# Kernel optimization log

Hardware: AMD Instinct MI355X
Metric: run time of the kernel (lower is better)

Reference implementation:

```python
import jax, jax.numpy as jnp
import numpy as np

N_NODES = 40000
N_EDGES = 640000
HIDDEN = 128
NUM_RBF = 50
CUTOFF = 10.0


def setup_inputs() -> dict:
    key = jax.random.key(0)
    ks = jax.random.split(key, 8)
    s = 1.0 / np.sqrt(HIDDEN)
    sf = 1.0 / np.sqrt(NUM_RBF)
    return {
        "x": jax.random.normal(ks[0], (N_NODES, HIDDEN), dtype=jnp.float32),
        "edge_index": jax.random.randint(ks[1], (2, N_EDGES), 0, N_NODES, dtype=jnp.int64),
        "edge_weight": jax.random.uniform(ks[2], (N_EDGES,), dtype=jnp.float32) * CUTOFF,
        "edge_attr": jax.random.normal(ks[3], (N_EDGES, NUM_RBF), dtype=jnp.float32),
        "W_f1": jax.random.normal(ks[4], (NUM_RBF, HIDDEN), dtype=jnp.float32) * sf,
        "b_f1": jnp.zeros((HIDDEN,), dtype=jnp.float32),
        "W_f2": jax.random.normal(ks[5], (HIDDEN, HIDDEN), dtype=jnp.float32) * s,
        "b_f2": jnp.zeros((HIDDEN,), dtype=jnp.float32),
        "W_in": jax.random.normal(ks[6], (HIDDEN, HIDDEN), dtype=jnp.float32) * s,
        "W_out": jax.random.normal(ks[7], (HIDDEN, HIDDEN), dtype=jnp.float32) * s,
        "b_out": jnp.zeros((HIDDEN,), dtype=jnp.float32),
        "W_lin": jax.random.normal(jax.random.fold_in(key, 7), (HIDDEN, HIDDEN), dtype=jnp.float32) * s,
        "b_lin": jnp.zeros((HIDDEN,), dtype=jnp.float32),
    }


def reference(x, edge_index, edge_weight, edge_attr,
              W_f1, b_f1, W_f2, b_f2, W_in, W_out, b_out, W_lin, b_lin):
    src = edge_index[0]
    dst = edge_index[1]
    n_nodes = x.shape[0]
    # filter network: MLP on RBF-expanded distances, modulated by cosine cutoff
    C = 0.5 * (jnp.cos(edge_weight * (jnp.pi / CUTOFF)) + 1.0)  # [E]
    Wf = jnp.tanh(edge_attr @ W_f1 + b_f1) @ W_f2 + b_f2        # [E, H]
    Wf = Wf * C[:, None]
    # cfconv: project, gather, filter-multiply, scatter-add, project
    h = x @ W_in                                                 # [N, H] (no bias)
    msg = h[src] * Wf                                            # [E, H]
    agg = jax.ops.segment_sum(msg, dst, num_segments=n_nodes)   # [N, H]
    out = agg @ W_out + b_out
    # interaction block tail: activation + linear
    out = jnp.tanh(out)
    return out @ W_lin + b_lin
```

## Files before the change

### kernel.cpp

```cpp
#include <hip/hip_runtime.h>
#include <hip/hip_bf16.h>

#define N_NODES 40000
#define N_EDGES 640000
#define HIDDEN  128
#define NUM_RBF 50
#define NBLK_SCAN 157

typedef __attribute__((ext_vector_type(8))) short bf16x8;
typedef __attribute__((ext_vector_type(4))) float f32x4;

#define WAVE_FENCE() do { asm volatile("" ::: "memory"); \
                          __builtin_amdgcn_sched_barrier(0); } while (0)

__device__ __forceinline__ short f2bf(float f) {
  __hip_bfloat16 h = __float2bfloat16(f);
  return (short)__builtin_bit_cast(unsigned short, h);
}
__device__ __forceinline__ float bf2f(unsigned short u) {
  unsigned int v = ((unsigned int)u) << 16;
  return __builtin_bit_cast(float, v);
}
__device__ __forceinline__ float bflo(unsigned int u) {
  return __builtin_bit_cast(float, u << 16);
}
__device__ __forceinline__ float bfhi(unsigned int u) {
  return __builtin_bit_cast(float, u & 0xffff0000u);
}
__device__ __forceinline__ unsigned int pack2bf(float a, float b) {
  return (unsigned int)(unsigned short)f2bf(a) |
         ((unsigned int)(unsigned short)f2bf(b) << 16);
}

__device__ __forceinline__ float fast_tanh(float x) {
  float e = __expf(2.0f * x);
  return 1.0f - 2.0f * __builtin_amdgcn_rcpf(e + 1.0f);
}

__device__ __forceinline__ f32x4 mfma16(bf16x8 a, bf16x8 b, f32x4 c) {
  return __builtin_amdgcn_mfma_f32_16x16x32_bf16(a, b, c, 0, 0, 0);
}

__device__ __forceinline__ bf16x8 load8_f32_bf16(const float* p) {
  const float4 v0 = ((const float4*)p)[0];
  const float4 v1 = ((const float4*)p)[1];
  bf16x8 r;
  r[0] = f2bf(v0.x); r[1] = f2bf(v0.y); r[2] = f2bf(v0.z); r[3] = f2bf(v0.w);
  r[4] = f2bf(v1.x); r[5] = f2bf(v1.y); r[6] = f2bf(v1.z); r[7] = f2bf(v1.w);
  return r;
}

__global__ __launch_bounds__(256) void hist_kernel(const int* __restrict__ ei,
                                                   int* __restrict__ hist) {
  int e = blockIdx.x * 256 + threadIdx.x;
  if (e < N_EDGES) atomicAdd(&hist[ei[N_EDGES + e]], 1);
}

__global__ __launch_bounds__(256) void scan1_kernel(const int* __restrict__ hist,
                                                    int* __restrict__ tmp,
                                                    int* __restrict__ bsum) {
  __shared__ int ls[256];
  const int t = threadIdx.x;
  const int i = blockIdx.x * 256 + t;
  int v = (i < N_NODES) ? hist[i] : 0;
  ls[t] = v;
  __syncthreads();
  for (int off = 1; off < 256; off <<= 1) {
    int u = (t >= off) ? ls[t - off] : 0;
    __syncthreads();
    ls[t] += u;
    __syncthreads();
  }
  if (i < N_NODES) tmp[i] = ls[t];
  if (t == 255) bsum[blockIdx.x] = ls[255];
}

__global__ __launch_bounds__(256) void scan2_kernel(const int* __restrict__ bsum,
                                                    int* __restrict__ bpfx,
                                                    int* __restrict__ row_start) {
  __shared__ int ls[256];
  const int t = threadIdx.x;
  int v = (t < NBLK_SCAN) ? bsum[t] : 0;
  ls[t] = v;
  __syncthreads();
  for (int off = 1; off < 256; off <<= 1) {
    int u = (t >= off) ? ls[t - off] : 0;
    __syncthreads();
    ls[t] += u;
    __syncthreads();
  }
  if (t < NBLK_SCAN) bpfx[t] = ls[t] - v;
  if (t == 255) row_start[N_NODES] = ls[255];
}

__global__ __launch_bounds__(256) void scan3_kernel(const int* __restrict__ hist,
                                                    const int* __restrict__ tmp,
                                                    const int* __restrict__ bpfx,
                                                    int* __restrict__ row_start,
                                                    int* __restrict__ cursor) {
  const int i = blockIdx.x * 256 + threadIdx.x;
  if (i < N_NODES) {
    int rs = tmp[i] - hist[i] + bpfx[blockIdx.x];
    row_start[i] = rs;
    cursor[i] = rs;
  }
}

__global__ __launch_bounds__(256) void perm_kernel(
    const int* __restrict__ ei, const float* __restrict__ ew,
    int* __restrict__ cursor,
    int* __restrict__ eSorted, int* __restrict__ srcSorted,
    float* __restrict__ Carr) {
  int e = blockIdx.x * 256 + threadIdx.x;
  if (e < N_EDGES) {
    int dst = ei[N_EDGES + e];
    int pos = atomicAdd(&cursor[dst], 1);
    eSorted[pos] = e;
    srcSorted[pos] = ei[e];
    Carr[pos] = 0.5f * (__cosf(ew[e] * 0.31415926535f) + 1.0f);
  }
}

__global__ __launch_bounds__(256) void hproj_kernel(
    const float* __restrict__ x, const float* __restrict__ W_in,
    unsigned short* __restrict__ hb)
{
  __shared__ __align__(16) unsigned short sWt[128 * 136];
  const int tid = threadIdx.x, wave = tid >> 6, lane = tid & 63;
  const int ln = lane & 15, grp = lane >> 4;
  const int r0 = blockIdx.x * 64;

  for (int idx = tid; idx < 128 * 128; idx += 256) {
    int k = idx >> 7, c = idx & 127;
    sWt[c * 136 + k] = f2bf(W_in[idx]);
  }
  __syncthreads();

  const size_t r = (size_t)r0 + wave * 16 + ln;
  f32x4 acc[8];
#pragma unroll
  for (int ct = 0; ct < 8; ++ct) acc[ct] = (f32x4){0.f, 0.f, 0.f, 0.f};
#pragma unroll
  for (int ks = 0; ks < 4; ++ks) {
    bf16x8 a = load8_f32_bf16(&x[r * 128 + ks * 32 + grp * 8]);
#pragma unroll
    for (int ct = 0; ct < 8; ++ct) {
      bf16x8 b = *(const bf16x8*)&sWt[(ct * 16 + ln) * 136 + ks * 32 + grp * 8];
      acc[ct] = mfma16(a, b, acc[ct]);
    }
  }
#pragma unroll
  for (int ct = 0; ct < 8; ++ct) {
#pragma unroll
    for (int i = 0; i < 4; ++i) {
      hb[(size_t)(r0 + wave * 16 + grp * 4 + i) * 128 + ct * 16 + ln] =
          (unsigned short)f2bf(acc[ct][i]);
    }
  }
}

__global__ __launch_bounds__(1024) void edgeagg_kernel(
    const float* __restrict__ edge_attr,
    const int*   __restrict__ eSorted,
    const int*   __restrict__ srcSorted,
    const float* __restrict__ Carr,
    const int*   __restrict__ row_start,
    const unsigned int* __restrict__ hb32,
    const float* __restrict__ W_f1, const float* __restrict__ b_f1,
    const float* __restrict__ W_f2, const float* __restrict__ b_f2,
    float* __restrict__ aggf)
{
  __shared__ __align__(16) unsigned short sW1t[128 * 72];
  __shared__ __align__(16) unsigned short sW2t[128 * 136];
  __shared__ __align__(16) unsigned short sT[256 * 136];
  __shared__ float sb1[128], sb2[128];

  const int tid = threadIdx.x, wave = tid >> 6, lane = tid & 63;
  const int ln = lane & 15, grp = lane >> 4;

  for (int idx = tid; idx < 128 * 64; idx += 1024) {
    int k = idx >> 7, c = idx & 127;
    sW1t[c * 72 + k] = (k < NUM_RBF) ? f2bf(W_f1[k * 128 + c]) : (short)0;
  }
  for (int idx = tid; idx < 128 * 128; idx += 1024) {
    int k = idx >> 7, c = idx & 127;
    sW2t[c * 136 + k] = f2bf(W_f2[idx]);
  }
  if (tid < 128) { sb1[tid] = b_f1[tid]; sb2[tid] = b_f2[tid]; }
  __syncthreads();

  const int gw = blockIdx.x * 16 + wave;
  const int nw = gridDim.x * 16;
  const int nGroups = N_NODES / 4;

  for (int ng = gw; ng < nGroups; ng += nw) {
    const int n0 = ng * 4;
    const int rs0 = row_start[n0],     rs1 = row_start[n0 + 1];
    const int rs2 = row_start[n0 + 2], rs3 = row_start[n0 + 3];
    const int rs4 = row_start[n0 + 4];

    float ax = 0.f, ay = 0.f;
    int cur = 0;
    int nb = rs1;

    for (int gb = rs0; gb < rs4; gb += 16) {
      const int lim = (rs4 - gb < 16) ? (rs4 - gb) : 16;

      unsigned int hv[16];
#pragma unroll
      for (int j = 0; j < 16; ++j) {
        int s = gb + j; if (s >= rs4) s = rs4 - 1;
        int src = srcSorted[s];
        hv[j] = hb32[(size_t)src * 64 + lane];
      }

      int sl = gb + ln; if (sl >= rs4) sl = rs4 - 1;
      const int eA = eSorted[sl];
      const float Cw = Carr[sl];
      const float* ap = edge_attr + (size_t)eA * NUM_RBF;
      bf16x8 a0, a1;
      {
        const float2* p = (const float2*)(ap + grp * 8);
        float2 v0 = p[0], v1 = p[1], v2 = p[2], v3 = p[3];
        a0[0] = f2bf(v0.x); a0[1] = f2bf(v0.y); a0[2] = f2bf(v1.x); a0[3] = f2bf(v1.y);
        a0[4] = f2bf(v2.x); a0[5] = f2bf(v2.y); a0[6] = f2bf(v3.x); a0[7] = f2bf(v3.y);
      }
      a1 = (bf16x8){0, 0, 0, 0, 0, 0, 0, 0};
      if (grp < 2) {
        const float2* p = (const float2*)(ap + 32 + grp * 8);
        float2 v0 = p[0], v1 = p[1], v2 = p[2], v3 = p[3];
        a1[0] = f2bf(v0.x); a1[1] = f2bf(v0.y); a1[2] = f2bf(v1.x); a1[3] = f2bf(v1.y);
        a1[4] = f2bf(v2.x); a1[5] = f2bf(v2.y); a1[6] = f2bf(v3.x); a1[7] = f2bf(v3.y);
      } else if (grp == 2) {
        const float2* p = (const float2*)(ap + 48);
        float2 v0 = p[0];
        a1[0] = f2bf(v0.x); a1[1] = f2bf(v0.y);
      }

#pragma unroll
      for (int ct = 0; ct < 8; ++ct) {
        f32x4 z = {0.f, 0.f, 0.f, 0.f};
        int c = ct * 16 + ln;
        bf16x8 b0 = *(const bf16x8*)&sW1t[c * 72 + grp * 8];
        bf16x8 b1 = *(const bf16x8*)&sW1t[c * 72 + 32 + grp * 8];
        z = mfma16(a0, b0, z);
        z = mfma16(a1, b1, z);
        float bias = sb1[c];
#pragma unroll
        for (int i = 0; i < 4; ++i) {
          int rl = wave * 16 + grp * 4 + i;
          sT[rl * 136 + c] = (unsigned short)f2bf(fast_tanh(z[i] + bias));
        }
      }
      WAVE_FENCE();

      bf16x8 af[4];
#pragma unroll
      for (int ks = 0; ks < 4; ++ks)
        af[ks] = *(const bf16x8*)&sT[(wave * 16 + ln) * 136 + ks * 32 + grp * 8];
      WAVE_FENCE();
#pragma unroll
      for (int ct = 0; ct < 8; ++ct) {
        f32x4 z = {0.f, 0.f, 0.f, 0.f};
        int c = ct * 16 + ln;
#pragma unroll
        for (int ks = 0; ks < 4; ++ks) {
          bf16x8 b = *(const bf16x8*)&sW2t[c * 136 + ks * 32 + grp * 8];
          z = mfma16(af[ks], b, z);
        }
        float bias = sb2[c];
#pragma unroll
        for (int i = 0; i < 4; ++i) {
          int rl = wave * 16 + grp * 4 + i;
          sT[rl * 136 + c] = (unsigned short)f2bf(z[i] + bias);
        }
      }
      WAVE_FENCE();

#pragma unroll
      for (int j = 0; j < 16; ++j) {
        if (j < lim) {
          while (cur < 4 && gb + j == nb) {
            ((float2*)aggf)[(size_t)(n0 + cur) * 64 + lane] =
                make_float2(ax, ay);
            ax = 0.f; ay = 0.f;
            ++cur;
            nb = (cur == 1) ? rs2 : (cur == 2) ? rs3 : rs4;
          }
          unsigned int w = *(const unsigned int*)&sT[(wave * 16 + j) * 136 + lane * 2];
          float C = __shfl(Cw, j, 64);
          ax = fmaf(C * bflo(w), bflo(hv[j]), ax);
          ay = fmaf(C * bfhi(w), bfhi(hv[j]), ay);
        }
      }
      WAVE_FENCE();
    }

    while (cur < 4) {
      ((float2*)aggf)[(size_t)(n0 + cur) * 64 + lane] = make_float2(ax, ay);
      ax = 0.f; ay = 0.f;
      ++cur;
    }
  }
}

__global__ __launch_bounds__(256) void tail_kernel(
    const float* agg,
    const float* __restrict__ W_out, const float* __restrict__ b_out,
    const float* __restrict__ W_lin, const float* __restrict__ b_lin,
    float* out)
{
  __shared__ __align__(16) unsigned short sWo[128 * 136];
  __shared__ __align__(16) unsigned short sWl[128 * 136];
  __shared__ __align__(16) unsigned short sT[64 * 136];
  __shared__ float sbo[128], sbl[128];
  const int tid = threadIdx.x, wave = tid >> 6, lane = tid & 63;
  const int ln = lane & 15, grp = lane >> 4;
  const int r0 = blockIdx.x * 64;

  for (int idx = tid; idx < 128 * 128; idx += 256) {
    int k = idx >> 7, c = idx & 127;
    sWo[c * 136 + k] = f2bf(W_out[idx]);
    sWl[c * 136 + k] = f2bf(W_lin[idx]);
  }
  if (tid < 128) { sbo[tid] = b_out[tid]; sbl[tid] = b_lin[tid]; }
  __syncthreads();

  const size_t r = (size_t)r0 + wave * 16 + ln;
  f32x4 acc[8];
#pragma unroll
  for (int ct = 0; ct < 8; ++ct) acc[ct] = (f32x4){0.f, 0.f, 0.f, 0.f};
#pragma unroll
  for (int ks = 0; ks < 4; ++ks) {
    bf16x8 a = load8_f32_bf16(&agg[r * 128 + ks * 32 + grp * 8]);
#pragma unroll
    for (int ct = 0; ct < 8; ++ct) {
      bf16x8 b = *(const bf16x8*)&sWo[(ct * 16 + ln) * 136 + ks * 32 + grp * 8];
      acc[ct] = mfma16(a, b, acc[ct]);
    }
  }
#pragma unroll
  for (int ct = 0; ct < 8; ++ct) {
    int c = ct * 16 + ln;
    float bias = sbo[c];
#pragma unroll
    for (int i = 0; i < 4; ++i) {
      int rl = wave * 16 + grp * 4 + i;
      sT[rl * 136 + c] = f2bf(fast_tanh(acc[ct][i] + bias));
    }
  }
  __syncthreads();

  bf16x8 af[4];
#pragma unroll
  for (int ks = 0; ks < 4; ++ks)
    af[ks] = *(const bf16x8*)&sT[(wave * 16 + ln) * 136 + ks * 32 + grp * 8];
  f32x4 acc2[8];
#pragma unroll
  for (int ct = 0; ct < 8; ++ct) {
    f32x4 z = {0.f, 0.f, 0.f, 0.f};
    int c = ct * 16 + ln;
#pragma unroll
    for (int ks = 0; ks < 4; ++ks) {
      bf16x8 b = *(const bf16x8*)&sWl[c * 136 + ks * 32 + grp * 8];
      z = mfma16(af[ks], b, z);
    }
    acc2[ct] = z;
  }
  __syncthreads();
#pragma unroll
  for (int ct = 0; ct < 8; ++ct) {
    int c = ct * 16 + ln;
    float bias = sbl[c];
#pragma unroll
    for (int i = 0; i < 4; ++i) {
      out[(size_t)(r0 + wave * 16 + grp * 4 + i) * 128 + c] = acc2[ct][i] + bias;
    }
  }
}

__global__ __launch_bounds__(256, 2) void edge_kernel(
    const float* __restrict__ edge_attr,
    const int*   __restrict__ edge_index,
    const float* __restrict__ edge_weight,
    const float* __restrict__ W_f1, const float* __restrict__ b_f1,
    const float* __restrict__ W_f2, const float* __restrict__ b_f2,
    const unsigned short* __restrict__ hb, float* __restrict__ agg)
{
  __shared__ __align__(16) unsigned short sW1t[128 * 72];
  __shared__ __align__(16) unsigned short sW2t[128 * 136];
  __shared__ __align__(16) unsigned short sT[64 * 136];
  __shared__ float sb1[128], sb2[128], sC[64];
  __shared__ int sSrc[64], sDst[64];

  const int tid = threadIdx.x, wave = tid >> 6, lane = tid & 63;
  const int ln = lane & 15, grp = lane >> 4;

  for (int idx = tid; idx < 128 * 64; idx += 256) {
    int k = idx >> 7, c = idx & 127;
    sW1t[c * 72 + k] = (k < NUM_RBF) ? f2bf(W_f1[k * 128 + c]) : (short)0;
  }
  for (int idx = tid; idx < 128 * 128; idx += 256) {
    int k = idx >> 7, c = idx & 127;
    sW2t[c * 136 + k] = f2bf(W_f2[idx]);
  }
  if (tid < 128) { sb1[tid] = b_f1[tid]; sb2[tid] = b_f2[tid]; }

  const int nTiles = N_EDGES / 64;
  for (int tile = blockIdx.x; tile < nTiles; tile += gridDim.x) {
    const int e0 = tile * 64;
    for (int idx = tid; idx < 64 * NUM_RBF; idx += 256) {
      int e = idx / NUM_RBF, k = idx - e * NUM_RBF;
      sT[e * 136 + k] = f2bf(edge_attr[(size_t)e0 * NUM_RBF + idx]);
    }
    for (int idx = tid; idx < 64 * 14; idx += 256) {
      int e = idx / 14, k = NUM_RBF + (idx - (idx / 14) * 14);
      sT[e * 136 + k] = 0;
    }
    if (tid < 64) {
      int e = e0 + tid;
      sC[tid] = 0.5f * (__cosf(edge_weight[e] * 0.31415926535f) + 1.0f);
      sSrc[tid] = edge_index[e];
      sDst[tid] = edge_index[N_EDGES + e];
    }
    __syncthreads();

    const int erow = wave * 16 + ln;
    bf16x8 a0 = *(const bf16x8*)&sT[erow * 136 + grp * 8];
    bf16x8 a1 = *(const bf16x8*)&sT[erow * 136 + 32 + grp * 8];
    __syncthreads();

    f32x4 acc[8];
#pragma unroll
    for (int ct = 0; ct < 8; ++ct) {
      f32x4 z = {0.f, 0.f, 0.f, 0.f};
      int c = ct * 16 + ln;
      bf16x8 b0 = *(const bf16x8*)&sW1t[c * 72 + grp * 8];
      bf16x8 b1 = *(const bf16x8*)&sW1t[c * 72 + 32 + grp * 8];
      z = mfma16(a0, b0, z);
      z = mfma16(a1, b1, z);
      acc[ct] = z;
    }
#pragma unroll
    for (int ct = 0; ct < 8; ++ct) {
      int c = ct * 16 + ln;
      float bias = sb1[c];
#pragma unroll
      for (int i = 0; i < 4; ++i) {
        int el = wave * 16 + grp * 4 + i;
        sT[el * 136 + c] = f2bf(fast_tanh(acc[ct][i] + bias));
      }
    }
    __syncthreads();

    bf16x8 af[4];
#pragma unroll
    for (int ks = 0; ks < 4; ++ks)
      af[ks] = *(const bf16x8*)&sT[erow * 136 + ks * 32 + grp * 8];
    f32x4 acc2[8];
#pragma unroll
    for (int ct = 0; ct < 8; ++ct) {
      f32x4 z = {0.f, 0.f, 0.f, 0.f};
      int c = ct * 16 + ln;
#pragma unroll
      for (int ks = 0; ks < 4; ++ks) {
        bf16x8 b = *(const bf16x8*)&sW2t[c * 136 + ks * 32 + grp * 8];
        z = mfma16(af[ks], b, z);
      }
      acc2[ct] = z;
    }
#pragma unroll
    for (int ct = 0; ct < 8; ++ct) {
      int c = ct * 16 + ln;
      float bias = sb2[c];
#pragma unroll
      for (int i = 0; i < 4; ++i) {
        int el = wave * 16 + grp * 4 + i;
        float wf = (acc2[ct][i] + bias) * sC[el];
        float m = bf2f(hb[(size_t)sSrc[el] * 128 + c]) * wf;
        atomicAdd(&agg[(size_t)sDst[el] * 128 + c], m);
      }
    }
    __syncthreads();
  }
}

extern "C" void kernel_launch(void* const* d_in, const int* in_sizes, int n_in,
                              void* d_out, int out_size, void* d_ws, size_t ws_size,
                              hipStream_t stream) {
  const float* x     = (const float*)d_in[0];
  const int*   ei    = (const int*)d_in[1];
  const float* ew    = (const float*)d_in[2];
  const float* ea    = (const float*)d_in[3];
  const float* W_f1  = (const float*)d_in[4];
  const float* b_f1  = (const float*)d_in[5];
  const float* W_f2  = (const float*)d_in[6];
  const float* b_f2  = (const float*)d_in[7];
  const float* W_in  = (const float*)d_in[8];
  const float* W_out = (const float*)d_in[9];
  const float* b_out = (const float*)d_in[10];
  const float* W_lin = (const float*)d_in[11];
  const float* b_lin = (const float*)d_in[12];

  const size_t HB_B  = (size_t)N_NODES * HIDDEN * 2;
  const size_t I_B   = (size_t)N_NODES * 4;
  const size_t RS_B  = ((size_t)(N_NODES + 1) * 4 + 15) & ~(size_t)15;
  const size_t SB_B  = 1024;
  const size_t POS_B = (size_t)N_EDGES * 4;
  const size_t NEED = HB_B + I_B + RS_B + I_B + I_B + SB_B + SB_B + 3 * POS_B;

  char* ws = (char*)d_ws;
  unsigned short* hb = (unsigned short*)ws;

  if (ws_size >= NEED) {
    char* q = ws + HB_B;
    int* hist      = (int*)q;                  q += I_B;
    int* row_start = (int*)q;                  q += RS_B;
    int* cursor    = (int*)q;                  q += I_B;
    int* tmp       = (int*)q;                  q += I_B;
    int* bsum      = (int*)q;                  q += SB_B;
    int* bpfx      = (int*)q;                  q += SB_B;
    int* eSorted   = (int*)q;                  q += POS_B;
    int* srcSorted = (int*)q;                  q += POS_B;
    float* Carr    = (float*)q;

    hipMemsetAsync(hist, 0, I_B, stream);
    hist_kernel<<<(N_EDGES + 255) / 256, 256, 0, stream>>>(ei, hist);
    scan1_kernel<<<NBLK_SCAN, 256, 0, stream>>>(hist, tmp, bsum);
    scan2_kernel<<<1, 256, 0, stream>>>(bsum, bpfx, row_start);
    scan3_kernel<<<NBLK_SCAN, 256, 0, stream>>>(hist, tmp, bpfx, row_start, cursor);
    perm_kernel<<<(N_EDGES + 255) / 256, 256, 0, stream>>>(ei, ew, cursor,
                                                           eSorted, srcSorted, Carr);
    hproj_kernel<<<N_NODES / 64, 256, 0, stream>>>(x, W_in, hb);
    edgeagg_kernel<<<256, 1024, 0, stream>>>(ea, eSorted, srcSorted, Carr,
                                             row_start,
                                             (const unsigned int*)hb,
                                             W_f1, b_f1, W_f2, b_f2,
                                             (float*)d_out);
    tail_kernel<<<N_NODES / 64, 256, 0, stream>>>((const float*)d_out,
                                                  W_out, b_out, W_lin, b_lin,
                                                  (float*)d_out);
  } else {
    float* agg = (float*)(ws + HB_B);
    hipMemsetAsync(agg, 0, (size_t)N_NODES * HIDDEN * 4, stream);
    hproj_kernel<<<N_NODES / 64, 256, 0, stream>>>(x, W_in, hb);
    edge_kernel<<<512, 256, 0, stream>>>(ea, ei, ew, W_f1, b_f1, W_f2, b_f2, hb, agg);
    tail_kernel<<<N_NODES / 64, 256, 0, stream>>>(agg, W_out, b_out, W_lin, b_lin,
                                                  (float*)d_out);
  }
}
```

Measured before the change: 227.6 us.

## Software-pipeline edge gathers by prefetching next 16-edge chunk into registers

Issues the gathers for the next 16-edge chunk (h rows, edge_attr, cutoff weight) before running the filter MLP and accumulation on the current chunk, then rotates the register buffers. This is meant to hide global-memory gather latency behind the MFMA and tanh work. It roughly doubles the live registers for the gathered data in a 1024-thread block, which could spill or lower occupancy.

```diff
diff --git a/kernel.cpp b/kernel.cpp
--- a/kernel.cpp
+++ b/kernel.cpp
@@ -158,6 +158,45 @@
     }
   }
 }
+
+#define LOADC_RAW(GB, HV, RA, RB, CW)                                        \
+  do {                                                                       \
+    _Pragma("unroll")                                                        \
+    for (int j_ = 0; j_ < 16; ++j_) {                                        \
+      int s_ = (GB) + j_; if (s_ >= rs4) s_ = rs4 - 1;                       \
+      int src_ = srcSorted[s_];                                              \
+      HV[j_] = hb32[(size_t)src_ * 64 + lane];                               \
+    }                                                                        \
+    int sl_ = (GB) + ln; if (sl_ >= rs4) sl_ = rs4 - 1;                      \
+    const int eA_ = eSorted[sl_];                                            \
+    CW = Carr[sl_];                                                          \
+    const float2* p0_ = (const float2*)(edge_attr + (size_t)eA_ * NUM_RBF + grp * 8); \
+    RA[0] = p0_[0]; RA[1] = p0_[1]; RA[2] = p0_[2]; RA[3] = p0_[3];          \
+    if (grp < 2) {                                                           \
+      const float2* p1_ = (const float2*)(edge_attr + (size_t)eA_ * NUM_RBF + 32 + grp * 8); \
+      RB[0] = p1_[0]; RB[1] = p1_[1]; RB[2] = p1_[2]; RB[3] = p1_[3];        \
+    } else if (grp == 2) {                                                   \
+      const float2* p1_ = (const float2*)(edge_attr + (size_t)eA_ * NUM_RBF + 48); \
+      RB[0] = p1_[0];                                                        \
+    }                                                                        \
+  } while (0)
+
+#define CONVC(RA, RB, A0, A1)                                                \
+  do {                                                                       \
+    A0[0] = f2bf(RA[0].x); A0[1] = f2bf(RA[0].y);                            \
+    A0[2] = f2bf(RA[1].x); A0[3] = f2bf(RA[1].y);                            \
+    A0[4] = f2bf(RA[2].x); A0[5] = f2bf(RA[2].y);                            \
+    A0[6] = f2bf(RA[3].x); A0[7] = f2bf(RA[3].y);                            \
+    A1 = (bf16x8){0, 0, 0, 0, 0, 0, 0, 0};                                   \
+    if (grp < 2) {                                                           \
+      A1[0] = f2bf(RB[0].x); A1[1] = f2bf(RB[0].y);                          \
+      A1[2] = f2bf(RB[1].x); A1[3] = f2bf(RB[1].y);                          \
+      A1[4] = f2bf(RB[2].x); A1[5] = f2bf(RB[2].y);                          \
+      A1[6] = f2bf(RB[3].x); A1[7] = f2bf(RB[3].y);                          \
+    } else if (grp == 2) {                                                   \
+      A1[0] = f2bf(RB[0].x); A1[1] = f2bf(RB[0].y);                          \
+    }                                                                        \
+  } while (0)
 
 __global__ __launch_bounds__(1024) void edgeagg_kernel(
     const float* __restrict__ edge_attr,
@@ -203,39 +242,23 @@
     int cur = 0;
     int nb = rs1;
 
+    unsigned int hv[16];
+    float2 rA[4], rB[4];
+    float Cw;
+    if (rs0 < rs4) LOADC_RAW(rs0, hv, rA, rB, Cw);
+
     for (int gb = rs0; gb < rs4; gb += 16) {
       const int lim = (rs4 - gb < 16) ? (rs4 - gb) : 16;
-
-      unsigned int hv[16];
-#pragma unroll
-      for (int j = 0; j < 16; ++j) {
-        int s = gb + j; if (s >= rs4) s = rs4 - 1;
-        int src = srcSorted[s];
-        hv[j] = hb32[(size_t)src * 64 + lane];
-      }
-
-      int sl = gb + ln; if (sl >= rs4) sl = rs4 - 1;
-      const int eA = eSorted[sl];
-      const float Cw = Carr[sl];
-      const float* ap = edge_attr + (size_t)eA * NUM_RBF;
+      const int gbn = gb + 16;
+      const bool hasNext = gbn < rs4;
+
+      unsigned int hvN[16];
+      float2 rAN[4], rBN[4];
+      float CwN;
+      if (hasNext) LOADC_RAW(gbn, hvN, rAN, rBN, CwN);
+
       bf16x8 a0, a1;
-      {
-        const float2* p = (const float2*)(ap + grp * 8);
-        float2 v0 = p[0], v1 = p[1], v2 = p[2], v3 = p[3];
-        a0[0] = f2bf(v0.x); a0[1] = f2bf(v0.y); a0[2] = f2bf(v1.x); a0[3] = f2bf(v1.y);
-        a0[4] = f2bf(v2.x); a0[5] = f2bf(v2.y); a0[6] = f2bf(v3.x); a0[7] = f2bf(v3.y);
-      }
-      a1 = (bf16x8){0, 0, 0, 0, 0, 0, 0, 0};
-      if (grp < 2) {
-        const float2* p = (const float2*)(ap + 32 + grp * 8);
-        float2 v0 = p[0], v1 = p[1], v2 = p[2], v3 = p[3];
-        a1[0] = f2bf(v0.x); a1[1] = f2bf(v0.y); a1[2] = f2bf(v1.x); a1[3] = f2bf(v1.y);
-        a1[4] = f2bf(v2.x); a1[5] = f2bf(v2.y); a1[6] = f2bf(v3.x); a1[7] = f2bf(v3.y);
-      } else if (grp == 2) {
-        const float2* p = (const float2*)(ap + 48);
-        float2 v0 = p[0];
-        a1[0] = f2bf(v0.x); a1[1] = f2bf(v0.y);
-      }
+      CONVC(rA, rB, a0, a1);
 
 #pragma unroll
       for (int ct = 0; ct < 8; ++ct) {
@@ -294,6 +317,14 @@
         }
       }
       WAVE_FENCE();
+
+      if (hasNext) {
+#pragma unroll
+        for (int j = 0; j < 16; ++j) hv[j] = hvN[j];
+        rA[0] = rAN[0]; rA[1] = rAN[1]; rA[2] = rAN[2]; rA[3] = rAN[3];
+        rB[0] = rBN[0]; rB[1] = rBN[1]; rB[2] = rBN[2]; rB[3] = rBN[3];
+        Cw = CwN;
+      }
     }
 
     while (cur < 4) {
```

Result: slower. 237.0 us (+4.1%).

## Fuse CSR build stages into one cooperative kernel with grid syncs

Applied to the files above, without the earlier changes.

Replaces the memset, histogram, three scan kernels and the permutation kernel with a single cooperative kernel of 256 blocks that separates the phases with grid-wide syncs. This removes five kernel launches and one memset along with their inter-kernel gaps. In exchange it runs the atomic-heavy histogram and permutation phases on a fixed, smaller grid using grid-stride loops, and it pays for each grid.sync barrier.

```diff
diff --git a/kernel.cpp b/kernel.cpp
--- a/kernel.cpp
+++ b/kernel.cpp
@@ -1,11 +1,14 @@
 #include <hip/hip_runtime.h>
 #include <hip/hip_bf16.h>
+#include <hip/hip_cooperative_groups.h>
 
 #define N_NODES 40000
 #define N_EDGES 640000
 #define HIDDEN  128
 #define NUM_RBF 50
 #define NBLK_SCAN 157
+
+namespace cg = cooperative_groups;
 
 typedef __attribute__((ext_vector_type(8))) short bf16x8;
 typedef __attribute__((ext_vector_type(4))) float f32x4;
@@ -50,69 +53,66 @@
   return r;
 }
 
-__global__ __launch_bounds__(256) void hist_kernel(const int* __restrict__ ei,
-                                                   int* __restrict__ hist) {
-  int e = blockIdx.x * 256 + threadIdx.x;
-  if (e < N_EDGES) atomicAdd(&hist[ei[N_EDGES + e]], 1);
-}
-
-__global__ __launch_bounds__(256) void scan1_kernel(const int* __restrict__ hist,
-                                                    int* __restrict__ tmp,
-                                                    int* __restrict__ bsum) {
+__global__ __launch_bounds__(256) void csr_build_kernel(
+    const int* __restrict__ ei, const float* __restrict__ ew,
+    int* __restrict__ hist, int* __restrict__ tmp,
+    int* __restrict__ bsum, int* __restrict__ bpfx,
+    int* __restrict__ row_start, int* __restrict__ cursor,
+    int* __restrict__ eSorted, int* __restrict__ srcSorted,
+    float* __restrict__ Carr)
+{
+  cg::grid_group grid = cg::this_grid();
   __shared__ int ls[256];
-  const int t = threadIdx.x;
-  const int i = blockIdx.x * 256 + t;
-  int v = (i < N_NODES) ? hist[i] : 0;
-  ls[t] = v;
-  __syncthreads();
-  for (int off = 1; off < 256; off <<= 1) {
-    int u = (t >= off) ? ls[t - off] : 0;
+  const int tid = threadIdx.x, bid = blockIdx.x;
+  const int gsize = gridDim.x * 256;
+  const int gtid = bid * 256 + tid;
+
+  for (int i = gtid; i < N_NODES; i += gsize) hist[i] = 0;
+  grid.sync();
+
+  for (int e = gtid; e < N_EDGES; e += gsize)
+    atomicAdd(&hist[ei[N_EDGES + e]], 1);
+  grid.sync();
+
+  if (bid < NBLK_SCAN) {
+    int i = bid * 256 + tid;
+    int v = (i < N_NODES) ? hist[i] : 0;
+    ls[tid] = v;
     __syncthreads();
-    ls[t] += u;
+    for (int off = 1; off < 256; off <<= 1) {
+      int u = (tid >= off) ? ls[tid - off] : 0;
+      __syncthreads();
+      ls[tid] += u;
+      __syncthreads();
+    }
+    if (i < N_NODES) tmp[i] = ls[tid];
+    if (tid == 255) bsum[bid] = ls[255];
+  }
+  grid.sync();
+
+  if (bid == 0) {
+    int v = (tid < NBLK_SCAN) ? bsum[tid] : 0;
+    ls[tid] = v;
     __syncthreads();
-  }
-  if (i < N_NODES) tmp[i] = ls[t];
-  if (t == 255) bsum[blockIdx.x] = ls[255];
-}
-
-__global__ __launch_bounds__(256) void scan2_kernel(const int* __restrict__ bsum,
-                                                    int* __restrict__ bpfx,
-                                                    int* __restrict__ row_start) {
-  __shared__ int ls[256];
-  const int t = threadIdx.x;
-  int v = (t < NBLK_SCAN) ? bsum[t] : 0;
-  ls[t] = v;
-  __syncthreads();
-  for (int off = 1; off < 256; off <<= 1) {
-    int u = (t >= off) ? ls[t - off] : 0;
-    __syncthreads();
-    ls[t] += u;
-    __syncthreads();
-  }
-  if (t < NBLK_SCAN) bpfx[t] = ls[t] - v;
-  if (t == 255) row_start[N_NODES] = ls[255];
-}
-
-__global__ __launch_bounds__(256) void scan3_kernel(const int* __restrict__ hist,
-                                                    const int* __restrict__ tmp,
-                                                    const int* __restrict__ bpfx,
-                                                    int* __restrict__ row_start,
-                                                    int* __restrict__ cursor) {
-  const int i = blockIdx.x * 256 + threadIdx.x;
-  if (i < N_NODES) {
-    int rs = tmp[i] - hist[i] + bpfx[blockIdx.x];
+    for (int off = 1; off < 256; off <<= 1) {
+      int u = (tid >= off) ? ls[tid - off] : 0;
+      __syncthreads();
+      ls[tid] += u;
+      __syncthreads();
+    }
+    if (tid < NBLK_SCAN) bpfx[tid] = ls[tid] - v;
+    if (tid == 255) row_start[N_NODES] = ls[255];
+  }
+  grid.sync();
+
+  for (int i = gtid; i < N_NODES; i += gsize) {
+    int rs = tmp[i] - hist[i] + bpfx[i >> 8];
     row_start[i] = rs;
     cursor[i] = rs;
   }
-}
-
-__global__ __launch_bounds__(256) void perm_kernel(
-    const int* __restrict__ ei, const float* __restrict__ ew,
-    int* __restrict__ cursor,
-    int* __restrict__ eSorted, int* __restrict__ srcSorted,
-    float* __restrict__ Carr) {
-  int e = blockIdx.x * 256 + threadIdx.x;
-  if (e < N_EDGES) {
+  grid.sync();
+
+  for (int e = gtid; e < N_EDGES; e += gsize) {
     int dst = ei[N_EDGES + e];
     int pos = atomicAdd(&cursor[dst], 1);
     eSorted[pos] = e;
@@ -524,13 +524,12 @@
     int* srcSorted = (int*)q;                  q += POS_B;
     float* Carr    = (float*)q;
 
-    hipMemsetAsync(hist, 0, I_B, stream);
-    hist_kernel<<<(N_EDGES + 255) / 256, 256, 0, stream>>>(ei, hist);
-    scan1_kernel<<<NBLK_SCAN, 256, 0, stream>>>(hist, tmp, bsum);
-    scan2_kernel<<<1, 256, 0, stream>>>(bsum, bpfx, row_start);
-    scan3_kernel<<<NBLK_SCAN, 256, 0, stream>>>(hist, tmp, bpfx, row_start, cursor);
-    perm_kernel<<<(N_EDGES + 255) / 256, 256, 0, stream>>>(ei, ew, cursor,
-                                                           eSorted, srcSorted, Carr);
+    void* args[] = {(void*)&ei, (void*)&ew, (void*)&hist, (void*)&tmp,
+                    (void*)&bsum, (void*)&bpfx, (void*)&row_start,
+                    (void*)&cursor, (void*)&eSorted, (void*)&srcSorted,
+                    (void*)&Carr};
+    hipLaunchCooperativeKernel((void*)csr_build_kernel, dim3(256), dim3(256),
+                               args, 0, stream);
     hproj_kernel<<<N_NODES / 64, 256, 0, stream>>>(x, W_in, hb);
     edgeagg_kernel<<<256, 1024, 0, stream>>>(ea, eSorted, srcSorted, Carr,
                                              row_start,
```

Result: slower. 365.6 us (+60.6%).
